# Kernel tuning notes

Hardware: AMD Instinct MI355X
Metric: run time of the kernel (lower is better)

The kernel has to match this reference:

```python
import jax, jax.numpy as jnp
import numpy as np

D_MODEL = 1024
N_HEADS = 16
HEAD_DIM = D_MODEL // N_HEADS


def setup_inputs() -> dict:
    key = jax.random.key(0)
    ks = jax.random.split(key, 7)
    b, s, l = 2, 2048, 8
    x = jax.random.normal(ks[0], (b, s, D_MODEL), dtype=jnp.float32)
    past_keys = jax.random.normal(ks[1], (b, N_HEADS, s, l, HEAD_DIM), dtype=jnp.float32)
    past_values = jax.random.normal(ks[2], (b, N_HEADS, s, l, HEAD_DIM), dtype=jnp.float32)
    sc = 1.0 / np.sqrt(D_MODEL)
    W_qkv = jax.random.normal(ks[3], (D_MODEL, 3 * D_MODEL), dtype=jnp.float32) * sc
    b_qkv = jnp.zeros((3 * D_MODEL,), dtype=jnp.float32)
    W_out = jax.random.normal(ks[4], (D_MODEL, D_MODEL), dtype=jnp.float32) * sc
    b_out = jnp.zeros((D_MODEL,), dtype=jnp.float32)
    return {"x": x, "past_keys": past_keys, "past_values": past_values,
            "W_qkv": W_qkv, "b_qkv": b_qkv, "W_out": W_out, "b_out": b_out}


def _split_heads(t):
    b, s, d = t.shape
    return t.reshape(b, s, N_HEADS, HEAD_DIM).transpose(0, 2, 1, 3)  # [b,h,s,hd]


def reference(x, past_keys, past_values, W_qkv, b_qkv, W_out, b_out):
    b, s, _ = x.shape
    qkv = x @ W_qkv + b_qkv  # [b,s,3d]
    q_row, k_row, v_row = jnp.split(qkv, 3, axis=-1)
    q = _split_heads(q_row)  # [b,h,s,hd]
    k = _split_heads(k_row)
    v = _split_heads(v_row)
    scale = 1.0 / jnp.sqrt(jnp.asarray(HEAD_DIM, dtype=x.dtype))
    token_scores = jnp.einsum('bhqd,bhkd->bhqk', q, k) * scale  # [b,h,s,s]
    causal = jnp.triu(jnp.ones((s, s), dtype=bool), k=1)
    token_scores = jnp.where(causal, -jnp.inf, token_scores)
    mem_scores = jnp.einsum('bhsd,bhsld->bhsl', q, past_keys) * scale  # [b,h,s,l]
    scores = jnp.concatenate([token_scores, mem_scores], axis=-1)  # [b,h,s,s+l]
    weights = jax.nn.softmax(scores, axis=-1)
    token_w = weights[..., :s]
    mem_w = weights[..., s:]
    token_ctx = jnp.einsum('bhqk,bhkd->bhqd', token_w, v)
    mem_ctx = jnp.einsum('bhsl,bhsld->bhsd', mem_w, past_values)
    out = token_ctx + mem_ctx  # [b,h,s,hd]
    out = out.transpose(0, 2, 1, 3).reshape(b, s, D_MODEL)
    out = out @ W_out + b_out
    return out, k, v
```

## Files before the change

### kernel.cpp

```cpp
#include <hip/hip_runtime.h>
#include <hip/hip_bf16.h>

#define D_MODEL 1024
#define N_HEADS 16
#define HEAD_DIM 64
#define BATCH 2
#define SEQ 2048
#define NMEM 8

#define SCALE_L2 0.18033688f

typedef __attribute__((ext_vector_type(8))) short vshort8;
typedef __attribute__((ext_vector_type(4))) short vshort4;
typedef __attribute__((ext_vector_type(4))) float f32x4;

static __device__ __forceinline__ short f2bf(float f) {
    unsigned u = __builtin_bit_cast(unsigned, f);
    unsigned r = u + 0x7fffu + ((u >> 16) & 1u);
    return (short)(r >> 16);
}
static __device__ __forceinline__ float bf2f(short s) {
    unsigned u = ((unsigned)(unsigned short)s) << 16;
    return __builtin_bit_cast(float, u);
}

static __device__ __forceinline__ f32x4 mfma16x16x32(vshort8 a, vshort8 b, f32x4 c) {
    return __builtin_amdgcn_mfma_f32_16x16x32_bf16(a, b, c, 0, 0, 0);
}

typedef const __attribute__((address_space(1))) char* gptr_t;
typedef __attribute__((address_space(3))) char* lptr_t;
static __device__ __forceinline__ void gload_lds16(const void* g, void* l) {
    __builtin_amdgcn_global_load_lds((gptr_t)g, (lptr_t)l, 16, 0, 0);
}

__global__ void cast_f32_bf16(const float* __restrict__ in, short* __restrict__ out, int n4) {
    int i = blockIdx.x * blockDim.x + threadIdx.x;
    if (i >= n4) return;
    float4 v = reinterpret_cast<const float4*>(in)[i];
    vshort4 o;
    o.x = f2bf(v.x); o.y = f2bf(v.y); o.z = f2bf(v.z); o.w = f2bf(v.w);
    reinterpret_cast<vshort4*>(out)[i] = o;
}

__global__ void transpose_cast(const float* __restrict__ in, short* __restrict__ out, int R, int C) {
    __shared__ float tile[32][33];
    int n0 = blockIdx.x * 32;
    int k0 = blockIdx.y * 32;
    int tx = threadIdx.x, ty = threadIdx.y;
    #pragma unroll
    for (int i = 0; i < 4; i++) {
        int r = ty + i * 8;
        tile[r][tx] = in[(k0 + r) * C + n0 + tx];
    }
    __syncthreads();
    #pragma unroll
    for (int i = 0; i < 4; i++) {
        int r = ty + i * 8;
        out[(n0 + r) * R + k0 + tx] = f2bf(tile[tx][r]);
    }
}

__global__ void transpose_cast_v(const float* __restrict__ in, short* __restrict__ out) {
    __shared__ float tile[32][33];
    int bh = blockIdx.z;
    int d0 = blockIdx.x * 32;
    int s0 = blockIdx.y * 32;
    const float* src = in + (size_t)bh * SEQ * 64;
    short* dst = out + (size_t)bh * 64 * SEQ;
    int tx = threadIdx.x, ty = threadIdx.y;
    #pragma unroll
    for (int i = 0; i < 4; i++) {
        int r = ty + i * 8;
        tile[r][tx] = src[(size_t)(s0 + r) * 64 + d0 + tx];
    }
    __syncthreads();
    #pragma unroll
    for (int i = 0; i < 4; i++) {
        int r = ty + i * 8;
        dst[(size_t)(d0 + r) * SEQ + s0 + tx] = f2bf(tile[tx][r]);
    }
}

#define BM 128
#define BN 128
#define BK 64

template<int EPI>
__global__ __launch_bounds__(256) void gemm_bf16(
    const short* __restrict__ A, const short* __restrict__ Bt,
    int M, int N, int K,
    const float* __restrict__ bias,
    float* __restrict__ Cout,
    short* __restrict__ Qb, short* __restrict__ Kb,
    float* __restrict__ k_out, float* __restrict__ v_out)
{
    __shared__ short As[BM][BK];
    __shared__ short Bs[BN][BK];
    int m0 = blockIdx.x * BM, n0 = blockIdx.y * BN;
    int tid = threadIdx.x;
    int wave = tid >> 6, lane = tid & 63;
    int wr = wave >> 1, wc = wave & 1;
    int lo = lane & 15, hi = lane >> 4;

    f32x4 acc[4][4];
    #pragma unroll
    for (int i = 0; i < 4; i++)
        #pragma unroll
        for (int j = 0; j < 4; j++)
            acc[i][j] = (f32x4){0.f, 0.f, 0.f, 0.f};

    int srow8 = wave * 8 + (lane >> 3);
    const char* Ab = (const char*)&As[0][0];
    const char* Bb = (const char*)&Bs[0][0];

    for (int k0 = 0; k0 < K; k0 += BK) {
        __syncthreads();
        #pragma unroll
        for (int r = 0; r < 4; r++) {
            int row = r * 32 + srow8;
            int sc8 = (((lane & 7) ^ (row & 7)) << 3);
            size_t dstoff = (size_t)r * 4096 + wave * 1024 + (size_t)(lane & 63) * 16;
            gload_lds16(&A[(size_t)(m0 + row) * K + k0 + sc8], (char*)Ab + dstoff);
            gload_lds16(&Bt[(size_t)(n0 + row) * K + k0 + sc8], (char*)Bb + dstoff);
        }
        __syncthreads();
        #pragma unroll
        for (int kk = 0; kk < 2; kk++) {
            vshort8 av[4], bv[4];
            #pragma unroll
            for (int fr = 0; fr < 4; fr++) {
                int ra = wr * 64 + fr * 16 + lo;
                av[fr] = *reinterpret_cast<const vshort8*>(
                    Ab + ra * 128 + (((kk * 4 + hi) ^ (ra & 7)) << 4));
            }
            #pragma unroll
            for (int fc = 0; fc < 4; fc++) {
                int rb = wc * 64 + fc * 16 + lo;
                bv[fc] = *reinterpret_cast<const vshort8*>(
                    Bb + rb * 128 + (((kk * 4 + hi) ^ (rb & 7)) << 4));
            }
            #pragma unroll
            for (int fr = 0; fr < 4; fr++)
                #pragma unroll
                for (int fc = 0; fc < 4; fc++)
                    acc[fr][fc] = mfma16x16x32(av[fr], bv[fc], acc[fr][fc]);
        }
    }

    #pragma unroll
    for (int fr = 0; fr < 4; fr++) {
        #pragma unroll
        for (int fc = 0; fc < 4; fc++) {
            int col = n0 + wc * 64 + fc * 16 + lo;
            float bb = bias[col];
            #pragma unroll
            for (int j = 0; j < 4; j++) {
                int row = m0 + wr * 64 + fr * 16 + hi * 4 + j;
                float val = acc[fr][fc][j] + bb;
                if (EPI == 0) {
                    Cout[row * N + col] = val;
                } else {
                    int sec = col >> 10, c = col & 1023;
                    int h = c >> 6, d = c & 63;
                    int b = row >> 11, s = row & 2047;
                    int idx = ((b * 16 + h) * 2048 + s) * 64 + d;
                    if (sec == 0) {
                        Qb[idx] = f2bf(val);
                    } else if (sec == 1) {
                        k_out[idx] = val;
                        Kb[idx] = f2bf(val);
                    } else {
                        v_out[idx] = val;
                    }
                }
            }
        }
    }
}

__global__ __launch_bounds__(256) void attn_kernel(
    const short* __restrict__ Qb, const short* __restrict__ Kb, const short* __restrict__ Vt,
    const float* __restrict__ pk, const float* __restrict__ pv,
    short* __restrict__ ctx)
{
    __shared__ short Ks[2][64][64];
    __shared__ short Vs[2][64][64];
    __shared__ short P[4][16][64];

    int bh = blockIdx.x;
    int y = blockIdx.y;
    int c = y & 7, m = y >> 3;
    int qblk = (m == 0) ? (31 - c) : (m == 1) ? c : (m == 2) ? (23 - c) : (8 + c);

    int b = bh >> 4, h = bh & 15;
    int wave = threadIdx.x >> 6, lane = threadIdx.x & 63;
    int lo = lane & 15, hi = lane >> 4;
    int qbase = qblk * 64 + wave * 16;

    const short* Qh = Qb + (size_t)bh * SEQ * 64;
    const short* Kh = Kb + (size_t)bh * SEQ * 64;
    const short* Vh = Vt + (size_t)bh * 64 * SEQ;

    char* Pw = (char*)&P[wave][0][0];
    float* wl = (float*)Pw;

    int st_sub  = lane >> 3;
    int st_csrc = (((lane & 7) ^ st_sub) << 4);

    #pragma unroll
    for (int rd = 0; rd < 2; rd++) {
        int tr = rd * 32 + wave * 8 + st_sub;
        gload_lds16((const char*)Kh + (((size_t)tr) << 7) + st_csrc,
                    ((char*)&Ks[0][0][0]) + rd * 4096 + wave * 1024);
        gload_lds16((const char*)Vh + (((size_t)tr) << 12) + st_csrc,
                    ((char*)&Vs[0][0][0]) + rd * 4096 + wave * 1024);
    }

    vshort8 aq[2];
    #pragma unroll
    for (int ks = 0; ks < 2; ks++)
        aq[ks] = *reinterpret_cast<const vshort8*>(&Qh[(size_t)(qbase + lo) * 64 + ks * 32 + hi * 8]);

    {
        int rm = lane >> 2, ml0 = lane & 3;
        size_t srow = (size_t)bh * SEQ + qbase + rm;
        const float4* pkA = reinterpret_cast<const float4*>(pk + (srow * 8 + ml0) * 64);
        const float4* pkB = pkA + 64;
        const short* qrow = Qh + (size_t)(qbase + rm) * 64;
        float dA = 0.f, dB = 0.f;
        #pragma unroll
        for (int t = 0; t < 16; t++) {
            float4 a4 = pkA[t];
            float4 b4 = pkB[t];
            vshort4 q4 = *reinterpret_cast<const vshort4*>(&qrow[t * 4]);
            float q0 = bf2f(q4.x), q1 = bf2f(q4.y), q2 = bf2f(q4.z), q3 = bf2f(q4.w);
            dA += q0 * a4.x + q1 * a4.y + q2 * a4.z + q3 * a4.w;
            dB += q0 * b4.x + q1 * b4.y + q2 * b4.z + q3 * b4.w;
        }
        wl[rm * 8 + ml0]     = dA * SCALE_L2;
        wl[rm * 8 + ml0 + 4] = dB * SCALE_L2;
    }
    asm volatile("s_waitcnt lgkmcnt(0)" ::: "memory");

    float m_r[4], ell[4];
    float ew[4][8];
    f32x4 o[4];
    #pragma unroll
    for (int j = 0; j < 4; j++) {
        int rr = hi * 4 + j;
        float mm = -3.0e38f;
        #pragma unroll
        for (int ml = 0; ml < 8; ml++) mm = fmaxf(mm, wl[rr * 8 + ml]);
        m_r[j] = mm;
        float e = 0.f;
        #pragma unroll
        for (int ml = 0; ml < 8; ml++) {
            float t = exp2f(wl[rr * 8 + ml] - mm);
            ew[j][ml] = t;
            e += t;
        }
        ell[j] = e;
    }
    #pragma unroll
    for (int g = 0; g < 4; g++) {
        #pragma unroll
        for (int j = 0; j < 4; j++) {
            size_t srow = (size_t)bh * SEQ + qbase + hi * 4 + j;
            const float* pvr = pv + srow * 8 * 64 + g * 16 + lo;
            float acc = 0.f;
            #pragma unroll
            for (int ml = 0; ml < 8; ml++)
                acc += ew[j][ml] * pvr[ml * 64];
            o[g][j] = acc;
        }
    }

    __syncthreads();

    int buf = 0;
    for (int kvt = 0; kvt <= qblk; kvt++) {
        if (kvt < qblk) {
            int kvbase = (kvt + 1) * 64;
            int nb = buf ^ 1;
            #pragma unroll
            for (int rd = 0; rd < 2; rd++) {
                int tr = rd * 32 + wave * 8 + st_sub;
                gload_lds16((const char*)Kh + (((size_t)(kvbase + tr)) << 7) + st_csrc,
                            ((char*)&Ks[nb][0][0]) + rd * 4096 + wave * 1024);
                gload_lds16((const char*)Vh + (((size_t)tr) << 12) + (size_t)kvbase * 2 + st_csrc,
                            ((char*)&Vs[nb][0][0]) + rd * 4096 + wave * 1024);
            }
        }
        int kvbase = kvt * 64;

        f32x4 sc[4];
        #pragma unroll
        for (int g = 0; g < 4; g++) {
            int kr = g * 16 + lo;
            const char* base = ((const char*)&Ks[buf][0][0]) + kr * 128;
            vshort8 bk0 = *reinterpret_cast<const vshort8*>(base + ((hi * 16) ^ ((kr & 7) << 4)));
            vshort8 bk1 = *reinterpret_cast<const vshort8*>(base + ((64 + hi * 16) ^ ((kr & 7) << 4)));
            f32x4 z = (f32x4){0.f, 0.f, 0.f, 0.f};
            z = mfma16x16x32(aq[0], bk0, z);
            sc[g] = mfma16x16x32(aq[1], bk1, z);
        }
        bool diag = (kvt == qblk);
        float p[4][4];
        float tm[4];
        #pragma unroll
        for (int j = 0; j < 4; j++) tm[j] = -3.0e38f;
        if (diag) {
            #pragma unroll
            for (int g = 0; g < 4; g++)
                #pragma unroll
                for (int j = 0; j < 4; j++) {
                    float sv = sc[g][j] * SCALE_L2;
                    if (kvbase + g * 16 + lo > qbase + hi * 4 + j) sv = -3.0e38f;
                    p[g][j] = sv;
                    tm[j] = fmaxf(tm[j], sv);
                }
        } else {
            #pragma unroll
            for (int g = 0; g < 4; g++)
                #pragma unroll
                for (int j = 0; j < 4; j++) {
                    float sv = sc[g][j] * SCALE_L2;
                    p[g][j] = sv;
                    tm[j] = fmaxf(tm[j], sv);
                }
        }
        #pragma unroll
        for (int j = 0; j < 4; j++) {
            tm[j] = fmaxf(tm[j], __shfl_xor(tm[j], 1));
            tm[j] = fmaxf(tm[j], __shfl_xor(tm[j], 2));
            tm[j] = fmaxf(tm[j], __shfl_xor(tm[j], 4));
            tm[j] = fmaxf(tm[j], __shfl_xor(tm[j], 8));
        }
        bool skip = (tm[0] <= m_r[0] + 8.f) && (tm[1] <= m_r[1] + 8.f) &&
                    (tm[2] <= m_r[2] + 8.f) && (tm[3] <= m_r[3] + 8.f);
        bool noresc = __all(skip);
        float fac[4], rs[4];
        #pragma unroll
        for (int j = 0; j < 4; j++) {
            if (noresc) {
                fac[j] = 1.f;
            } else {
                float mn = fmaxf(m_r[j], tm[j]);
                fac[j] = exp2f(m_r[j] - mn);
                m_r[j] = mn;
            }
            rs[j] = 0.f;
        }
        #pragma unroll
        for (int g = 0; g < 4; g++)
            #pragma unroll
            for (int j = 0; j < 4; j++) {
                p[g][j] = exp2f(p[g][j] - m_r[j]);
                rs[j] += p[g][j];
            }
        #pragma unroll
        for (int j = 0; j < 4; j++) {
            rs[j] += __shfl_xor(rs[j], 1);
            rs[j] += __shfl_xor(rs[j], 2);
            rs[j] += __shfl_xor(rs[j], 4);
            rs[j] += __shfl_xor(rs[j], 8);
            ell[j] = ell[j] * fac[j] + rs[j];
        }
        if (!noresc) {
            #pragma unroll
            for (int g = 0; g < 4; g++)
                #pragma unroll
                for (int j = 0; j < 4; j++)
                    o[g][j] *= fac[j];
        }

        #pragma unroll
        for (int g = 0; g < 4; g++)
            #pragma unroll
            for (int j = 0; j < 4; j++) {
                int r = hi * 4 + j;
                *reinterpret_cast<short*>(Pw + r * 128 +
                    ((((2 * g + (lo >> 3)) ^ (r & 7)) << 4) + 2 * (lo & 7))) = f2bf(p[g][j]);
            }

        vshort8 ap0 = *reinterpret_cast<const vshort8*>(Pw + lo * 128 + ((hi ^ (lo & 7)) << 4));
        vshort8 ap1 = *reinterpret_cast<const vshort8*>(Pw + lo * 128 + (((4 + hi) ^ (lo & 7)) << 4));
        #pragma unroll
        for (int g = 0; g < 4; g++) {
            int vr = g * 16 + lo;
            const char* base = ((const char*)&Vs[buf][0][0]) + vr * 128;
            vshort8 bv0 = *reinterpret_cast<const vshort8*>(base + ((hi * 16) ^ ((vr & 7) << 4)));
            vshort8 bv1 = *reinterpret_cast<const vshort8*>(base + ((64 + hi * 16) ^ ((vr & 7) << 4)));
            o[g] = mfma16x16x32(ap0, bv0, o[g]);
            o[g] = mfma16x16x32(ap1, bv1, o[g]);
        }

        __syncthreads();
        buf ^= 1;
    }

    #pragma unroll
    for (int g = 0; g < 4; g++)
        #pragma unroll
        for (int j = 0; j < 4; j++) {
            int s = qbase + hi * 4 + j;
            float val = o[g][j] / ell[j];
            ctx[(size_t)(b * SEQ + s) * D_MODEL + h * 64 + g * 16 + lo] = f2bf(val);
        }
}

extern "C" void kernel_launch(void* const* d_in, const int* in_sizes, int n_in,
                              void* d_out, int out_size, void* d_ws, size_t ws_size,
                              hipStream_t stream) {
    const float* x    = (const float*)d_in[0];
    const float* pk   = (const float*)d_in[1];
    const float* pv   = (const float*)d_in[2];
    const float* Wqkv = (const float*)d_in[3];
    const float* bqkv = (const float*)d_in[4];
    const float* Wout = (const float*)d_in[5];
    const float* bout = (const float*)d_in[6];

    float* out   = (float*)d_out;
    float* k_out = out + 4194304;
    float* v_out = out + 8388608;

    char* ws = (char*)d_ws;
    short* Xb    = (short*)(ws);
    short* Wqkvt = (short*)(ws + (size_t)(8  << 20));
    short* Woutt = (short*)(ws + (size_t)(14 << 20));
    short* Qb    = (short*)(ws + (size_t)(16 << 20));
    short* Kb    = (short*)(ws + (size_t)(24 << 20));
    short* Vt    = (short*)(ws + (size_t)(32 << 20));
    short* ctx   = Xb;

    cast_f32_bf16<<<4096, 256, 0, stream>>>(x, Xb, 4194304 / 4);
    dim3 tb(32, 8);
    transpose_cast<<<dim3(96, 32), tb, 0, stream>>>(Wqkv, Wqkvt, 1024, 3072);
    transpose_cast<<<dim3(32, 32), tb, 0, stream>>>(Wout, Woutt, 1024, 1024);

    gemm_bf16<1><<<dim3(32, 24), 256, 0, stream>>>(
        Xb, Wqkvt, 4096, 3072, 1024, bqkv,
        nullptr, Qb, Kb, k_out, v_out);

    transpose_cast_v<<<dim3(2, 64, 32), tb, 0, stream>>>(v_out, Vt);

    attn_kernel<<<dim3(32, 32), 256, 0, stream>>>(Qb, Kb, Vt, pk, pv, ctx);

    gemm_bf16<0><<<dim3(32, 8), 256, 0, stream>>>(
        ctx, Woutt, 4096, 1024, 1024, bout,
        out, nullptr, nullptr, nullptr, nullptr);
}
```

Baseline: 470.4 us.

## Split long causal query blocks into two KV chunks with combine pass

Query blocks 16-31 now have their KV range split into two chunks processed by separate workgroups, producing partial outputs plus max and sum values in scratch buffers. A new combine kernel merges them with log-sum-exp rescaling. Short blocks run unsplit, which evens out per-workgroup work and raises the grid from 1024 to 1536 blocks. In exchange it adds an extra launch, fp32 partial-output traffic, and reuses the output and weight workspace buffers as scratch.

```diff
diff --git a/kernel.cpp b/kernel.cpp
--- a/kernel.cpp
+++ b/kernel.cpp
@@ -179,19 +179,25 @@
     }
 }
 
-__global__ __launch_bounds__(256) void attn_kernel(
+__global__ __launch_bounds__(256) void attn_chunk(
     const short* __restrict__ Qb, const short* __restrict__ Kb, const short* __restrict__ Vt,
     const float* __restrict__ pk, const float* __restrict__ pv,
-    short* __restrict__ ctx)
+    short* __restrict__ ctx, float* __restrict__ part_o, float* __restrict__ part_ml)
 {
     __shared__ short Ks[2][64][64];
     __shared__ short Vs[2][64][64];
     __shared__ short P[4][16][64];
 
-    int bh = blockIdx.x;
-    int y = blockIdx.y;
-    int c = y & 7, m = y >> 3;
-    int qblk = (m == 0) ? (31 - c) : (m == 1) ? c : (m == 2) ? (23 - c) : (8 + c);
+    int x = blockIdx.x, bh = blockIdx.y;
+    int qblk, chunk, nchunks, kv_begin, kv_end;
+    if (x < 16) {
+        qblk = 16 + x; chunk = 0; nchunks = 2; kv_begin = 0; kv_end = 16;
+    } else if (x < 32) {
+        qblk = 15 - (x - 16); chunk = 0; nchunks = 1; kv_begin = 0; kv_end = qblk + 1;
+    } else {
+        qblk = 31 - (x - 32); chunk = 1; nchunks = 2; kv_begin = 16; kv_end = qblk + 1;
+    }
+    bool do_mem = (chunk == nchunks - 1);
 
     int b = bh >> 4, h = bh & 15;
     int wave = threadIdx.x >> 6, lane = threadIdx.x & 63;
@@ -208,13 +214,16 @@
     int st_sub  = lane >> 3;
     int st_csrc = (((lane & 7) ^ st_sub) << 4);
 
-    #pragma unroll
-    for (int rd = 0; rd < 2; rd++) {
-        int tr = rd * 32 + wave * 8 + st_sub;
-        gload_lds16((const char*)Kh + (((size_t)tr) << 7) + st_csrc,
-                    ((char*)&Ks[0][0][0]) + rd * 4096 + wave * 1024);
-        gload_lds16((const char*)Vh + (((size_t)tr) << 12) + st_csrc,
-                    ((char*)&Vs[0][0][0]) + rd * 4096 + wave * 1024);
+    {
+        int kvbase = kv_begin * 64;
+        #pragma unroll
+        for (int rd = 0; rd < 2; rd++) {
+            int tr = rd * 32 + wave * 8 + st_sub;
+            gload_lds16((const char*)Kh + (((size_t)(kvbase + tr)) << 7) + st_csrc,
+                        ((char*)&Ks[0][0][0]) + rd * 4096 + wave * 1024);
+            gload_lds16((const char*)Vh + (((size_t)tr) << 12) + (size_t)kvbase * 2 + st_csrc,
+                        ((char*)&Vs[0][0][0]) + rd * 4096 + wave * 1024);
+        }
     }
 
     vshort8 aq[2];
@@ -222,65 +231,74 @@
     for (int ks = 0; ks < 2; ks++)
         aq[ks] = *reinterpret_cast<const vshort8*>(&Qh[(size_t)(qbase + lo) * 64 + ks * 32 + hi * 8]);
 
-    {
-        int rm = lane >> 2, ml0 = lane & 3;
-        size_t srow = (size_t)bh * SEQ + qbase + rm;
-        const float4* pkA = reinterpret_cast<const float4*>(pk + (srow * 8 + ml0) * 64);
-        const float4* pkB = pkA + 64;
-        const short* qrow = Qh + (size_t)(qbase + rm) * 64;
-        float dA = 0.f, dB = 0.f;
-        #pragma unroll
-        for (int t = 0; t < 16; t++) {
-            float4 a4 = pkA[t];
-            float4 b4 = pkB[t];
-            vshort4 q4 = *reinterpret_cast<const vshort4*>(&qrow[t * 4]);
-            float q0 = bf2f(q4.x), q1 = bf2f(q4.y), q2 = bf2f(q4.z), q3 = bf2f(q4.w);
-            dA += q0 * a4.x + q1 * a4.y + q2 * a4.z + q3 * a4.w;
-            dB += q0 * b4.x + q1 * b4.y + q2 * b4.z + q3 * b4.w;
-        }
-        wl[rm * 8 + ml0]     = dA * SCALE_L2;
-        wl[rm * 8 + ml0 + 4] = dB * SCALE_L2;
-    }
-    asm volatile("s_waitcnt lgkmcnt(0)" ::: "memory");
-
     float m_r[4], ell[4];
-    float ew[4][8];
     f32x4 o[4];
-    #pragma unroll
-    for (int j = 0; j < 4; j++) {
-        int rr = hi * 4 + j;
-        float mm = -3.0e38f;
-        #pragma unroll
-        for (int ml = 0; ml < 8; ml++) mm = fmaxf(mm, wl[rr * 8 + ml]);
-        m_r[j] = mm;
-        float e = 0.f;
-        #pragma unroll
-        for (int ml = 0; ml < 8; ml++) {
-            float t = exp2f(wl[rr * 8 + ml] - mm);
-            ew[j][ml] = t;
-            e += t;
-        }
-        ell[j] = e;
-    }
-    #pragma unroll
-    for (int g = 0; g < 4; g++) {
+
+    if (do_mem) {
+        {
+            int rm = lane >> 2, ml0 = lane & 3;
+            size_t srow = (size_t)bh * SEQ + qbase + rm;
+            const float4* pkA = reinterpret_cast<const float4*>(pk + (srow * 8 + ml0) * 64);
+            const float4* pkB = pkA + 64;
+            const short* qrow = Qh + (size_t)(qbase + rm) * 64;
+            float dA = 0.f, dB = 0.f;
+            #pragma unroll
+            for (int t = 0; t < 16; t++) {
+                float4 a4 = pkA[t];
+                float4 b4 = pkB[t];
+                vshort4 q4 = *reinterpret_cast<const vshort4*>(&qrow[t * 4]);
+                float q0 = bf2f(q4.x), q1 = bf2f(q4.y), q2 = bf2f(q4.z), q3 = bf2f(q4.w);
+                dA += q0 * a4.x + q1 * a4.y + q2 * a4.z + q3 * a4.w;
+                dB += q0 * b4.x + q1 * b4.y + q2 * b4.z + q3 * b4.w;
+            }
+            wl[rm * 8 + ml0]     = dA * SCALE_L2;
+            wl[rm * 8 + ml0 + 4] = dB * SCALE_L2;
+        }
+        asm volatile("s_waitcnt lgkmcnt(0)" ::: "memory");
+
+        float ew[4][8];
         #pragma unroll
         for (int j = 0; j < 4; j++) {
-            size_t srow = (size_t)bh * SEQ + qbase + hi * 4 + j;
-            const float* pvr = pv + srow * 8 * 64 + g * 16 + lo;
-            float acc = 0.f;
-            #pragma unroll
-            for (int ml = 0; ml < 8; ml++)
-                acc += ew[j][ml] * pvr[ml * 64];
-            o[g][j] = acc;
-        }
+            int rr = hi * 4 + j;
+            float mm = -3.0e38f;
+            #pragma unroll
+            for (int ml = 0; ml < 8; ml++) mm = fmaxf(mm, wl[rr * 8 + ml]);
+            m_r[j] = mm;
+            float e = 0.f;
+            #pragma unroll
+            for (int ml = 0; ml < 8; ml++) {
+                float t = exp2f(wl[rr * 8 + ml] - mm);
+                ew[j][ml] = t;
+                e += t;
+            }
+            ell[j] = e;
+        }
+        #pragma unroll
+        for (int gq = 0; gq < 4; gq++) {
+            #pragma unroll
+            for (int j = 0; j < 4; j++) {
+                size_t srow = (size_t)bh * SEQ + qbase + hi * 4 + j;
+                const float* pvr = pv + srow * 8 * 64 + gq * 16 + lo;
+                float acc = 0.f;
+                #pragma unroll
+                for (int ml = 0; ml < 8; ml++)
+                    acc += ew[j][ml] * pvr[ml * 64];
+                o[gq][j] = acc;
+            }
+        }
+    } else {
+        #pragma unroll
+        for (int j = 0; j < 4; j++) { m_r[j] = -3.0e38f; ell[j] = 0.f; }
+        #pragma unroll
+        for (int gq = 0; gq < 4; gq++)
+            o[gq] = (f32x4){0.f, 0.f, 0.f, 0.f};
     }
 
     __syncthreads();
 
     int buf = 0;
-    for (int kvt = 0; kvt <= qblk; kvt++) {
-        if (kvt < qblk) {
+    for (int kvt = kv_begin; kvt < kv_end; kvt++) {
+        if (kvt + 1 < kv_end) {
             int kvbase = (kvt + 1) * 64;
             int nb = buf ^ 1;
             #pragma unroll
@@ -296,14 +314,14 @@
 
         f32x4 sc[4];
         #pragma unroll
-        for (int g = 0; g < 4; g++) {
-            int kr = g * 16 + lo;
+        for (int gq = 0; gq < 4; gq++) {
+            int kr = gq * 16 + lo;
             const char* base = ((const char*)&Ks[buf][0][0]) + kr * 128;
             vshort8 bk0 = *reinterpret_cast<const vshort8*>(base + ((hi * 16) ^ ((kr & 7) << 4)));
             vshort8 bk1 = *reinterpret_cast<const vshort8*>(base + ((64 + hi * 16) ^ ((kr & 7) << 4)));
             f32x4 z = (f32x4){0.f, 0.f, 0.f, 0.f};
             z = mfma16x16x32(aq[0], bk0, z);
-            sc[g] = mfma16x16x32(aq[1], bk1, z);
+            sc[gq] = mfma16x16x32(aq[1], bk1, z);
         }
         bool diag = (kvt == qblk);
         float p[4][4];
@@ -312,21 +330,21 @@
         for (int j = 0; j < 4; j++) tm[j] = -3.0e38f;
         if (diag) {
             #pragma unroll
-            for (int g = 0; g < 4; g++)
+            for (int gq = 0; gq < 4; gq++)
                 #pragma unroll
                 for (int j = 0; j < 4; j++) {
-                    float sv = sc[g][j] * SCALE_L2;
-                    if (kvbase + g * 16 + lo > qbase + hi * 4 + j) sv = -3.0e38f;
-                    p[g][j] = sv;
+                    float sv = sc[gq][j] * SCALE_L2;
+                    if (kvbase + gq * 16 + lo > qbase + hi * 4 + j) sv = -3.0e38f;
+                    p[gq][j] = sv;
                     tm[j] = fmaxf(tm[j], sv);
                 }
         } else {
             #pragma unroll
-            for (int g = 0; g < 4; g++)
+            for (int gq = 0; gq < 4; gq++)
                 #pragma unroll
                 for (int j = 0; j < 4; j++) {
-                    float sv = sc[g][j] * SCALE_L2;
-                    p[g][j] = sv;
+                    float sv = sc[gq][j] * SCALE_L2;
+                    p[gq][j] = sv;
                     tm[j] = fmaxf(tm[j], sv);
                 }
         }
@@ -353,11 +371,11 @@
             rs[j] = 0.f;
         }
         #pragma unroll
-        for (int g = 0; g < 4; g++)
+        for (int gq = 0; gq < 4; gq++)
             #pragma unroll
             for (int j = 0; j < 4; j++) {
-                p[g][j] = exp2f(p[g][j] - m_r[j]);
-                rs[j] += p[g][j];
+                p[gq][j] = exp2f(p[gq][j] - m_r[j]);
+                rs[j] += p[gq][j];
             }
         #pragma unroll
         for (int j = 0; j < 4; j++) {
@@ -369,45 +387,106 @@
         }
         if (!noresc) {
             #pragma unroll
-            for (int g = 0; g < 4; g++)
+            for (int gq = 0; gq < 4; gq++)
                 #pragma unroll
                 for (int j = 0; j < 4; j++)
-                    o[g][j] *= fac[j];
-        }
-
-        #pragma unroll
-        for (int g = 0; g < 4; g++)
+                    o[gq][j] *= fac[j];
+        }
+
+        #pragma unroll
+        for (int gq = 0; gq < 4; gq++)
             #pragma unroll
             for (int j = 0; j < 4; j++) {
                 int r = hi * 4 + j;
                 *reinterpret_cast<short*>(Pw + r * 128 +
-                    ((((2 * g + (lo >> 3)) ^ (r & 7)) << 4) + 2 * (lo & 7))) = f2bf(p[g][j]);
+                    ((((2 * gq + (lo >> 3)) ^ (r & 7)) << 4) + 2 * (lo & 7))) = f2bf(p[gq][j]);
             }
 
         vshort8 ap0 = *reinterpret_cast<const vshort8*>(Pw + lo * 128 + ((hi ^ (lo & 7)) << 4));
         vshort8 ap1 = *reinterpret_cast<const vshort8*>(Pw + lo * 128 + (((4 + hi) ^ (lo & 7)) << 4));
         #pragma unroll
-        for (int g = 0; g < 4; g++) {
-            int vr = g * 16 + lo;
+        for (int gq = 0; gq < 4; gq++) {
+            int vr = gq * 16 + lo;
             const char* base = ((const char*)&Vs[buf][0][0]) + vr * 128;
             vshort8 bv0 = *reinterpret_cast<const vshort8*>(base + ((hi * 16) ^ ((vr & 7) << 4)));
             vshort8 bv1 = *reinterpret_cast<const vshort8*>(base + ((64 + hi * 16) ^ ((vr & 7) << 4)));
-            o[g] = mfma16x16x32(ap0, bv0, o[g]);
-            o[g] = mfma16x16x32(ap1, bv1, o[g]);
+            o[gq] = mfma16x16x32(ap0, bv0, o[gq]);
+            o[gq] = mfma16x16x32(ap1, bv1, o[gq]);
         }
 
         __syncthreads();
         buf ^= 1;
     }
 
-    #pragma unroll
-    for (int g = 0; g < 4; g++)
-        #pragma unroll
-        for (int j = 0; j < 4; j++) {
-            int s = qbase + hi * 4 + j;
-            float val = o[g][j] / ell[j];
-            ctx[(size_t)(b * SEQ + s) * D_MODEL + h * 64 + g * 16 + lo] = f2bf(val);
-        }
+    if (nchunks == 1) {
+        #pragma unroll
+        for (int gq = 0; gq < 4; gq++)
+            #pragma unroll
+            for (int j = 0; j < 4; j++) {
+                int s = qbase + hi * 4 + j;
+                float val = o[gq][j] / ell[j];
+                ctx[(size_t)(b * SEQ + s) * D_MODEL + h * 64 + gq * 16 + lo] = f2bf(val);
+            }
+    } else {
+        int slot = bh * 32 + (qblk - 16) * 2 + chunk;
+        float* po = part_o + (size_t)slot * 4096;
+        #pragma unroll
+        for (int gq = 0; gq < 4; gq++)
+            #pragma unroll
+            for (int j = 0; j < 4; j++)
+                po[(wave * 16 + hi * 4 + j) * 64 + gq * 16 + lo] = o[gq][j];
+        if (lo == 0) {
+            float* pml = part_ml + (size_t)slot * 128;
+            #pragma unroll
+            for (int j = 0; j < 4; j++) {
+                pml[wave * 16 + hi * 4 + j] = m_r[j];
+                pml[64 + wave * 16 + hi * 4 + j] = ell[j];
+            }
+        }
+    }
+}
+
+__global__ __launch_bounds__(256) void attn_combine(
+    const float* __restrict__ part_o, const float* __restrict__ part_ml,
+    short* __restrict__ ctx)
+{
+    int qblk = 16 + blockIdx.x;
+    int bh = blockIdx.y;
+    int slot0 = bh * 32 + (qblk - 16) * 2;
+
+    int tid = threadIdx.x;
+    int row = tid >> 2;
+    int colb = (tid & 3) * 16;
+
+    float m0 = part_ml[(size_t)slot0 * 128 + row];
+    float l0 = part_ml[(size_t)slot0 * 128 + 64 + row];
+    float m1 = part_ml[(size_t)(slot0 + 1) * 128 + row];
+    float l1 = part_ml[(size_t)(slot0 + 1) * 128 + 64 + row];
+    float mstar = fmaxf(m0, m1);
+    float s0 = exp2f(m0 - mstar);
+    float s1 = exp2f(m1 - mstar);
+    float inv = 1.f / (s0 * l0 + s1 * l1);
+
+    const float4* p0 = reinterpret_cast<const float4*>(
+        part_o + (size_t)slot0 * 4096 + row * 64 + colb);
+    const float4* p1 = reinterpret_cast<const float4*>(
+        part_o + (size_t)(slot0 + 1) * 4096 + row * 64 + colb);
+
+    int b = bh >> 4, h = bh & 15;
+    int srow = qblk * 64 + row;
+    short out16[16];
+    #pragma unroll
+    for (int t = 0; t < 4; t++) {
+        float4 a = p0[t];
+        float4 c = p1[t];
+        out16[t * 4 + 0] = f2bf((s0 * a.x + s1 * c.x) * inv);
+        out16[t * 4 + 1] = f2bf((s0 * a.y + s1 * c.y) * inv);
+        out16[t * 4 + 2] = f2bf((s0 * a.z + s1 * c.z) * inv);
+        out16[t * 4 + 3] = f2bf((s0 * a.w + s1 * c.w) * inv);
+    }
+    short* dst = ctx + (size_t)(b * SEQ + srow) * D_MODEL + h * 64 + colb;
+    *reinterpret_cast<vshort8*>(dst) = *reinterpret_cast<vshort8*>(&out16[0]);
+    *reinterpret_cast<vshort8*>(dst + 8) = *reinterpret_cast<vshort8*>(&out16[8]);
 }
 
 extern "C" void kernel_launch(void* const* d_in, const int* in_sizes, int n_in,
@@ -426,13 +505,16 @@
     float* v_out = out + 8388608;
 
     char* ws = (char*)d_ws;
-    short* Xb    = (short*)(ws);
-    short* Wqkvt = (short*)(ws + (size_t)(8  << 20));
-    short* Woutt = (short*)(ws + (size_t)(14 << 20));
-    short* Qb    = (short*)(ws + (size_t)(16 << 20));
-    short* Kb    = (short*)(ws + (size_t)(24 << 20));
-    short* Vt    = (short*)(ws + (size_t)(32 << 20));
-    short* ctx   = Xb;
+    short* Xb      = (short*)(ws);
+    short* Wqkvt   = (short*)(ws + (size_t)(8  << 20));
+    short* Woutt   = (short*)(ws + (size_t)(14 << 20));
+    short* Qb      = (short*)(ws + (size_t)(16 << 20));
+    short* Kb      = (short*)(ws + (size_t)(24 << 20));
+    short* Vt      = (short*)(ws + (size_t)(32 << 20));
+    short* ctx     = Xb;
+
+    float* part_o  = out;
+    float* part_ml = (float*)Wqkvt;
 
     cast_f32_bf16<<<4096, 256, 0, stream>>>(x, Xb, 4194304 / 4);
     dim3 tb(32, 8);
@@ -445,7 +527,8 @@
 
     transpose_cast_v<<<dim3(2, 64, 32), tb, 0, stream>>>(v_out, Vt);
 
-    attn_kernel<<<dim3(32, 32), 256, 0, stream>>>(Qb, Kb, Vt, pk, pv, ctx);
+    attn_chunk<<<dim3(48, 32), 256, 0, stream>>>(Qb, Kb, Vt, pk, pv, ctx, part_o, part_ml);
+    attn_combine<<<dim3(16, 32), 256, 0, stream>>>(part_o, part_ml, ctx);
 
     gemm_bf16<0><<<dim3(32, 8), 256, 0, stream>>>(
         ctx, Woutt, 4096, 1024, 1024, bout,
```

After: 473.3 us. Within noise of the previous version (+0.6%).
